# Optimization experiments

Hardware: AMD Instinct MI355X
Metric: run time of the kernel (lower is better)

Reference implementation:

```python
import jax, jax.numpy as jnp
import numpy as np

IOU_THRESHOLD = 0.5
NEG_POS_RATIO = 3
FOCAL_ALPHA = 0.25
FOCAL_GAMMA = 2.0
LOC_LOSS_WEIGHT = 1.0
EPS = 1e-7


def _make_boxes(key, shape):
    # valid xyxy boxes in [0,1]
    k1, k2 = jax.random.split(key)
    xy1 = jax.random.uniform(k1, shape[:-1] + (2,)) * 0.8
    wh = jax.random.uniform(k2, shape[:-1] + (2,)) * 0.2 + 0.01
    return jnp.concatenate([xy1, xy1 + wh], axis=-1)


def setup_inputs() -> dict:
    key = jax.random.key(0)
    k1, k2, k3 = jax.random.split(key, 3)
    B, A, G = 16, 65536, 64
    bbox_pred = _make_boxes(k1, (B, A, 4))
    conf_pred = jax.random.normal(k2, (B, A), dtype=jnp.float32)
    gt_boxes = _make_boxes(k3, (B, G, 4))
    return {"bbox_pred": bbox_pred, "conf_pred": conf_pred, "gt_boxes": gt_boxes}


def box_iou(a, b):
    # a: [A,4], b: [G,4] xyxy -> [A,G]
    area_a = (a[:, 2] - a[:, 0]) * (a[:, 3] - a[:, 1])
    area_b = (b[:, 2] - b[:, 0]) * (b[:, 3] - b[:, 1])
    lt = jnp.maximum(a[:, None, :2], b[None, :, :2])
    rb = jnp.minimum(a[:, None, 2:], b[None, :, 2:])
    wh = jnp.clip(rb - lt, 0.0)
    inter = wh[..., 0] * wh[..., 1]
    return inter / (area_a[:, None] + area_b[None, :] - inter + EPS)


def diou_loss(pred, gt):
    # pred, gt: [N,4] xyxy -> [N]
    area_p = (pred[:, 2] - pred[:, 0]) * (pred[:, 3] - pred[:, 1])
    area_g = (gt[:, 2] - gt[:, 0]) * (gt[:, 3] - gt[:, 1])
    lt = jnp.maximum(pred[:, :2], gt[:, :2])
    rb = jnp.minimum(pred[:, 2:], gt[:, 2:])
    wh = jnp.clip(rb - lt, 0.0)
    inter = wh[:, 0] * wh[:, 1]
    iou = inter / (area_p + area_g - inter + EPS)
    cp = (pred[:, :2] + pred[:, 2:]) * 0.5
    cg = (gt[:, :2] + gt[:, 2:]) * 0.5
    center_d2 = jnp.sum((cp - cg) ** 2, axis=-1)
    elt = jnp.minimum(pred[:, :2], gt[:, :2])
    erb = jnp.maximum(pred[:, 2:], gt[:, 2:])
    diag2 = jnp.sum((erb - elt) ** 2, axis=-1) + EPS
    return 1.0 - iou + center_d2 / diag2


def focal_loss(logits, targets):
    # BCE-with-logits, stable
    ce = jnp.maximum(logits, 0.0) - logits * targets + jnp.log1p(jnp.exp(-jnp.abs(logits)))
    p = jax.nn.sigmoid(logits)
    p_t = jnp.clip(p * targets + (1 - p) * (1 - targets), EPS, 1.0 - EPS)
    focal_w = jax.lax.stop_gradient((1.0 - p_t) ** FOCAL_GAMMA)
    alpha_t = FOCAL_ALPHA * targets + (1 - FOCAL_ALPHA) * (1 - targets)
    return alpha_t * focal_w * ce


def _per_image(bb, cp, gt):
    A = cp.shape[0]
    ious = box_iou(bb, gt)                     # [A,G]
    best_gt_iou = ious.max(axis=1)             # [A]
    best_gt_idx = ious.argmax(axis=1)          # [A]
    best_anchor_idx = ious.argmax(axis=0)      # [G]
    pos = best_gt_iou > IOU_THRESHOLD
    pos = pos.at[best_anchor_idx].set(True)    # force best anchor per GT positive
    posf = pos.astype(cp.dtype)
    num_pos = posf.sum()

    matched_gt = gt[best_gt_idx]               # [A,4]
    loc = (diou_loss(bb, matched_gt) * posf).sum() * LOC_LOSS_WEIGHT

    fl = focal_loss(cp, posf)                  # [A]
    pos_sum = (fl * posf).sum()
    # hard-negative mining: descending sort of negative losses, keep top k
    neg_vals = jnp.where(pos, -1.0, fl)        # focal loss >= 0, so -1 sentinel
    sorted_neg = -jnp.sort(-neg_vals)
    num_neg = jnp.minimum(A - num_pos, num_pos * NEG_POS_RATIO)
    keep = jnp.arange(A) < num_neg
    neg_sum = jnp.where(keep, sorted_neg, 0.0).sum()
    conf = (pos_sum + neg_sum) / jnp.maximum(num_pos + num_neg, 1.0)
    return loc, conf, num_pos


def reference(bbox_pred, conf_pred, gt_boxes):
    loc, conf, npos = jax.vmap(_per_image)(bbox_pred, conf_pred, gt_boxes)
    total_pos = jnp.maximum(npos.sum(), 1.0)
    avg_loc = loc.sum() / total_pos
    avg_conf = conf.sum() / total_pos
    return avg_loc + avg_conf, avg_conf, avg_loc
```

## Files before the change

kernel.cpp:

```cpp
#include <hip/hip_runtime.h>
#include <stdint.h>

#define A_N 65536
#define B_N 16
#define G_N 64
#define FEPS 1e-7f

#define NBIN 2048
#define SHB  21

__device__ __forceinline__ float focal_one(float l, float tt) {
  float e  = __expf(-fabsf(l));
  float sp = __logf(1.0f + e);
  bool  tp = tt > 0.5f;
  float ce = (tp ? fmaxf(-l, 0.0f) : fmaxf(l, 0.0f)) + sp;
  float inv = __builtin_amdgcn_rcpf(1.0f + e);
  float sig = (l >= 0.0f) ? inv : e * inv;
  float om  = tp ? (1.0f - sig) : sig;
  om = fminf(fmaxf(om, FEPS), 1.0f - FEPS);
  float alpha = tp ? 0.25f : 0.75f;
  return alpha * om * om * ce;
}

__device__ __forceinline__ float diou_one(float4 p, float4 q) {
  float ap = (p.z - p.x) * (p.w - p.y);
  float ag = (q.z - q.x) * (q.w - q.y);
  float ix1 = fmaxf(p.x, q.x), iy1 = fmaxf(p.y, q.y);
  float ix2 = fminf(p.z, q.z), iy2 = fminf(p.w, q.w);
  float iw = fmaxf(ix2 - ix1, 0.0f), ih = fmaxf(iy2 - iy1, 0.0f);
  float inter = iw * ih;
  float iou = inter / (ap + ag - inter + FEPS);
  float cpx = (p.x + p.z) * 0.5f, cpy = (p.y + p.w) * 0.5f;
  float cgx = (q.x + q.z) * 0.5f, cgy = (q.y + q.w) * 0.5f;
  float dx = cpx - cgx, dy = cpy - cgy;
  float cd2 = dx * dx + dy * dy;
  float ex1 = fminf(p.x, q.x), ey1 = fminf(p.y, q.y);
  float ex2 = fmaxf(p.z, q.z), ey2 = fmaxf(p.w, q.w);
  float ddx = ex2 - ex1, ddy = ey2 - ey1;
  float dg2 = ddx * ddx + ddy * ddy + FEPS;
  return 1.0f - iou + cd2 / dg2;
}

__global__ void dl_init(uint32_t* __restrict__ histz) {
  int i = blockIdx.x * 1024 + threadIdx.x;
  histz[i] = 0u;
}

__global__ __launch_bounds__(256) void dl_pass1(
    const float4* __restrict__ bbox, const float* __restrict__ conf,
    const float4* __restrict__ gt,
    uint8_t* __restrict__ best_idx, uint32_t* __restrict__ negkey,
    unsigned long long* __restrict__ gt_part,
    uint32_t* __restrict__ hist_cnt, float* __restrict__ hist_sum,
    float* __restrict__ part_loc, float* __restrict__ part_fl, float* __restrict__ part_np) {
  const int img = blockIdx.y;
  const int bx  = blockIdx.x;
  const int t   = threadIdx.x;
  const int wave = t >> 6, lane = t & 63;
  const int a = bx * 256 + t;
  const int idx = img * A_N + a;

  __shared__ float4 sg2[2 * G_N];
  __shared__ float  sga2[2 * G_N];
  __shared__ unsigned long long spart[4][G_N];
  __shared__ uint32_t hc[NBIN];
  __shared__ float    hs[NBIN];
  __shared__ float sl[4], sf[4], sn[4];

  for (int i = t; i < NBIN; i += 256) { hc[i] = 0u; hs[i] = 0.f; }
  if (t < G_N) {
    float4 q0 = gt[img * G_N + t];
    float qa0 = __fmul_rn(__fsub_rn(q0.z, q0.x), __fsub_rn(q0.w, q0.y));
    sg2[t] = q0;  sg2[t + G_N] = q0;
    sga2[t] = qa0; sga2[t + G_N] = qa0;
  }
  __syncthreads();

  float4 p = bbox[idx];
  float pa = __fmul_rn(__fsub_rn(p.z, p.x), __fsub_rn(p.w, p.y));
  float l = conf[idx];

  float posm = -1.f;
  uint32_t rowkey = 0u;
  uint32_t colkey = 0u;
  uint32_t tb = 63u - (uint32_t)lane;
  const int rotsrc = (lane + 1) & 63;
  const uint32_t lanecomp = 63u - (uint32_t)lane;

  #pragma unroll 8
  for (int j = 0; j < G_N; ++j) {
    float4 q = sg2[lane + j];
    float qa = sga2[lane + j];
    float ix1 = fmaxf(p.x, q.x), iy1 = fmaxf(p.y, q.y);
    float ix2 = fminf(p.z, q.z), iy2 = fminf(p.w, q.w);
    float iw = fmaxf(__fsub_rn(ix2, ix1), 0.f);
    float ih = fmaxf(__fsub_rn(iy2, iy1), 0.f);
    float inter = __fmul_rn(iw, ih);
    float den = __fadd_rn(__fsub_rn(__fadd_rn(pa, qa), inter), FEPS);
    posm = fmaxf(posm, __fmaf_rn(2.f, inter, -den));
    float ratio = inter * __builtin_amdgcn_rcpf(den);
    uint32_t base = __float_as_uint(ratio) & 0xFFFFFFC0u;
    uint32_t rkey = base | tb;
    if (rkey > rowkey) rowkey = rkey;
    uint32_t ckey = base | lanecomp;
    if (ckey > colkey) colkey = ckey;
    colkey = __shfl(colkey, rotsrc);
    tb = (tb - 1u) & 63u;
  }

  const bool pos = posm > 0.f;
  const int bidx = 63 - (int)(rowkey & 63u);
  best_idx[idx] = (uint8_t)bidx;

  float fl = focal_one(l, pos ? 1.0f : 0.0f);
  negkey[idx] = pos ? 0u : __float_as_uint(fl);
  float locv = pos ? diou_one(p, sg2[bidx]) : 0.0f;
  if (!pos) {
    uint32_t kb = __float_as_uint(fl);
    atomicAdd(&hc[kb >> SHB], 1u);
    atomicAdd(&hs[kb >> SHB], fl);
  }

  uint32_t winlane = 63u - (colkey & 63u);
  uint32_t ganchor = (uint32_t)(bx * 256 + wave * 64) + winlane;
  unsigned long long wkey = ((unsigned long long)(colkey & 0xFFFFFFC0u) << 32)
                          | (unsigned)~ganchor;
  spart[wave][lane] = wkey;

  float flp = pos ? fl : 0.0f;
  float np1 = pos ? 1.0f : 0.0f;
  float lv = locv;
  for (int o = 32; o; o >>= 1) {
    lv  += __shfl_down(lv, o);
    flp += __shfl_down(flp, o);
    np1 += __shfl_down(np1, o);
  }
  if (lane == 0) { sl[wave] = lv; sf[wave] = flp; sn[wave] = np1; }
  __syncthreads();

  for (int i = t; i < NBIN; i += 256) {
    uint32_t c = hc[i];
    if (c) {
      atomicAdd(&hist_cnt[img * NBIN + i], c);
      atomicAdd(&hist_sum[img * NBIN + i], hs[i]);
    }
  }
  if (t < G_N) {
    unsigned long long m = spart[0][t];
    if (spart[1][t] > m) m = spart[1][t];
    if (spart[2][t] > m) m = spart[2][t];
    if (spart[3][t] > m) m = spart[3][t];
    gt_part[(((size_t)(img << 8) | bx) << 6) | t] = m;
  }
  if (t == 0) {
    const int pi = img * 256 + bx;
    part_loc[pi] = sl[0] + sl[1] + sl[2] + sl[3];
    part_fl[pi]  = sf[0] + sf[1] + sf[2] + sf[3];
    part_np[pi]  = sn[0] + sn[1] + sn[2] + sn[3];
  }
}

__global__ __launch_bounds__(1024) void dl_select(
    uint32_t* negkey,
    const unsigned long long* __restrict__ gt_part,
    const uint32_t* __restrict__ hist_cnt, const float* __restrict__ hist_sum,
    const float* __restrict__ part_loc, const float* __restrict__ part_fl,
    const float* __restrict__ part_np,
    const float4* __restrict__ bbox, const float* __restrict__ conf,
    const float4* __restrict__ gt, const uint8_t* __restrict__ best_idx,
    float* __restrict__ acc) {
  const int img = blockIdx.x;
  const int t = threadIdx.x;
  uint32_t* negk = negkey + (size_t)img * A_N;
  const uint4* k4 = (const uint4*)negk;
  const int N4 = A_N / 4;

  __shared__ uint32_t cnt[NBIN];
  __shared__ float    bsum[NBIN];
  __shared__ uint32_t hc2[NBIN];
  __shared__ float    hs2[NBIN];
  __shared__ uint32_t cnt3[1024];
  __shared__ unsigned long long gred[16][G_N];
  __shared__ float s3[3][4];
  __shared__ float redf[16];
  __shared__ float np_sh, psum_sh, loc_sh, sstar_sh, sstar2_sh, negsum_sh;
  __shared__ float fix_l, fix_f, fix_n;
  __shared__ uint32_t bstar_sh, cstar_sh, b2_sh, c2_sh, j3_sh, c3_sh;

  for (int i = t; i < NBIN; i += 1024) {
    cnt[i]  = hist_cnt[img * NBIN + i];
    bsum[i] = hist_sum[img * NBIN + i];
    hc2[i] = 0u; hs2[i] = 0.f;
  }
  cnt3[t] = 0u;
  {
    const int g = t & 63, ch = t >> 6;
    unsigned long long m = 0ull;
    #pragma unroll 4
    for (int j = 0; j < 16; ++j) {
      unsigned long long v = gt_part[(((size_t)(img << 8) | (ch * 16 + j)) << 6) | g];
      if (v > m) m = v;
    }
    gred[ch][g] = m;
  }
  float lv = 0.f, fv = 0.f, nv = 0.f;
  if (t < 256) {
    lv = part_loc[img * 256 + t];
    fv = part_fl[img * 256 + t];
    nv = part_np[img * 256 + t];
  }
  for (int o = 32; o; o >>= 1) {
    lv += __shfl_down(lv, o);
    fv += __shfl_down(fv, o);
    nv += __shfl_down(nv, o);
  }
  if (t < 256 && (t & 63) == 0) { s3[0][t >> 6] = lv; s3[1][t >> 6] = fv; s3[2][t >> 6] = nv; }
  __syncthreads();

  if (t < 64) {
    unsigned long long m = gred[0][t];
    #pragma unroll
    for (int c = 1; c < 16; ++c) if (gred[c][t] > m) m = gred[c][t];
    uint32_t a = ~(uint32_t)(m & 0xFFFFFFFFull);
    uint32_t old = atomicExch(&negk[a], 0u);
    float dl = 0.f, df = 0.f, dn = 0.f;
    if (old != 0u) {
      dn = 1.f;
      float fln = __uint_as_float(old);
      uint32_t bin = old >> SHB;
      atomicSub(&cnt[bin], 1u);
      atomicAdd(&bsum[bin], -fln);
      const int ai = img * A_N + (int)a;
      df = focal_one(conf[ai], 1.0f);
      dl = diou_one(bbox[ai], gt[img * G_N + best_idx[ai]]);
    }
    for (int o = 32; o; o >>= 1) {
      dl += __shfl_down(dl, o);
      df += __shfl_down(df, o);
      dn += __shfl_down(dn, o);
    }
    if (t == 0) { fix_l = dl; fix_f = df; fix_n = dn; }
  }
  __syncthreads();

  if (t == 0) {
    loc_sh  = s3[0][0] + s3[0][1] + s3[0][2] + s3[0][3] + fix_l;
    psum_sh = s3[1][0] + s3[1][1] + s3[1][2] + s3[1][3] + fix_f;
    np_sh   = s3[2][0] + s3[2][1] + s3[2][2] + s3[2][3] + fix_n;
    negsum_sh = 0.f;
  }
  __syncthreads();

  const int np = (int)(np_sh + 0.5f);
  const int k = min(A_N - np, 3 * np);

  if (k > 0) {
    if (t < 64) {
      const int CH = NBIN / 64;
      const int lob = NBIN - CH * (t + 1);
      uint32_t csum = 0;
      for (int b = lob; b < lob + CH; ++b) csum += cnt[b];
      uint32_t pre = csum;
      for (int o = 1; o < 64; o <<= 1) { uint32_t u = __shfl_up(pre, o); if (t >= o) pre += u; }
      uint32_t run = pre - csum;
      for (int b = lob + CH - 1; b >= lob; --b) {
        uint32_t c = cnt[b];
        if (run < (uint32_t)k && run + c >= (uint32_t)k) { bstar_sh = (uint32_t)b; cstar_sh = run; }
        run += c;
      }
    }
    __syncthreads();
    const uint32_t bstar = bstar_sh;
    const uint32_t cbin = cnt[bstar];
    const uint32_t r = (uint32_t)k - cstar_sh;

    float s = 0.f;
    for (int i = t; i < NBIN; i += 1024) if (i > (int)bstar) s += bsum[i];
    for (int o = 32; o; o >>= 1) s += __shfl_down(s, o);
    if ((t & 63) == 0) redf[t >> 6] = s;
    __syncthreads();
    if (t == 0) {
      float ss = 0.f;
      #pragma unroll
      for (int w = 0; w < 16; ++w) ss += redf[w];
      sstar_sh = ss;
    }
    __syncthreads();

    if (r == cbin) {
      if (t == 0) negsum_sh = sstar_sh + bsum[bstar];
    } else {
      for (int i = t; i < N4; i += 1024) {
        uint4 v = k4[i];
        if (v.x != 0u && (v.x >> SHB) == bstar) { atomicAdd(&hc2[(v.x >> 10) & 2047u], 1u); atomicAdd(&hs2[(v.x >> 10) & 2047u], __uint_as_float(v.x)); }
        if (v.y != 0u && (v.y >> SHB) == bstar) { atomicAdd(&hc2[(v.y >> 10) & 2047u], 1u); atomicAdd(&hs2[(v.y >> 10) & 2047u], __uint_as_float(v.y)); }
        if (v.z != 0u && (v.z >> SHB) == bstar) { atomicAdd(&hc2[(v.z >> 10) & 2047u], 1u); atomicAdd(&hs2[(v.z >> 10) & 2047u], __uint_as_float(v.z)); }
        if (v.w != 0u && (v.w >> SHB) == bstar) { atomicAdd(&hc2[(v.w >> 10) & 2047u], 1u); atomicAdd(&hs2[(v.w >> 10) & 2047u], __uint_as_float(v.w)); }
      }
      __syncthreads();

      if (t < 64) {
        const int CH = NBIN / 64;
        const int lob = NBIN - CH * (t + 1);
        uint32_t csum = 0;
        for (int b = lob; b < lob + CH; ++b) csum += hc2[b];
        uint32_t pre = csum;
        for (int o = 1; o < 64; o <<= 1) { uint32_t u = __shfl_up(pre, o); if (t >= o) pre += u; }
        uint32_t run = pre - csum;
        for (int b = lob + CH - 1; b >= lob; --b) {
          uint32_t c = hc2[b];
          if (run < r && run + c >= r) { b2_sh = (uint32_t)b; c2_sh = run; }
          run += c;
        }
      }
      __syncthreads();
      const uint32_t b2 = b2_sh;
      const uint32_t cbin2 = hc2[b2];
      const uint32_t r3 = r - c2_sh;

      float s2 = 0.f;
      for (int i = t; i < NBIN; i += 1024) if (i > (int)b2) s2 += hs2[i];
      for (int o = 32; o; o >>= 1) s2 += __shfl_down(s2, o);
      if ((t & 63) == 0) redf[t >> 6] = s2;
      __syncthreads();
      if (t == 0) {
        float ss = 0.f;
        #pragma unroll
        for (int w = 0; w < 16; ++w) ss += redf[w];
        sstar2_sh = ss;
      }
      __syncthreads();

      if (r3 == cbin2) {
        if (t == 0) negsum_sh = sstar_sh + sstar2_sh + hs2[b2];
      } else {
        const uint32_t top22 = (bstar << 11) | b2;
        for (int i = t; i < N4; i += 1024) {
          uint4 v = k4[i];
          if (v.x != 0u && (v.x >> 10) == top22) atomicAdd(&cnt3[v.x & 1023u], 1u);
          if (v.y != 0u && (v.y >> 10) == top22) atomicAdd(&cnt3[v.y & 1023u], 1u);
          if (v.z != 0u && (v.z >> 10) == top22) atomicAdd(&cnt3[v.z & 1023u], 1u);
          if (v.w != 0u && (v.w >> 10) == top22) atomicAdd(&cnt3[v.w & 1023u], 1u);
        }
        __syncthreads();

        if (t < 64) {
          const int CH = 1024 / 64;
          const int lob = 1024 - CH * (t + 1);
          uint32_t csum = 0;
          for (int b = lob; b < lob + CH; ++b) csum += cnt3[b];
          uint32_t pre = csum;
          for (int o = 1; o < 64; o <<= 1) { uint32_t u = __shfl_up(pre, o); if (t >= o) pre += u; }
          uint32_t run = pre - csum;
          for (int b = lob + CH - 1; b >= lob; --b) {
            uint32_t c = cnt3[b];
            if (run < r3 && run + c >= r3) { j3_sh = (uint32_t)b; c3_sh = run; }
            run += c;
          }
        }
        __syncthreads();
        const uint32_t j3 = j3_sh;
        const uint32_t hibits = (bstar << SHB) | (b2 << 10);

        float s3v = 0.f;
        if (t > (int)j3 && cnt3[t]) {
          s3v = (float)cnt3[t] * __uint_as_float(hibits | (uint32_t)t);
        }
        for (int o = 32; o; o >>= 1) s3v += __shfl_down(s3v, o);
        if ((t & 63) == 0) redf[t >> 6] = s3v;
        __syncthreads();
        if (t == 0) {
          float ss = 0.f;
          #pragma unroll
          for (int w = 0; w < 16; ++w) ss += redf[w];
          negsum_sh = sstar_sh + sstar2_sh + ss
                    + (float)(int)(r3 - c3_sh) * __uint_as_float(hibits | j3);
        }
      }
    }
  }
  __syncthreads();
  if (t == 0) {
    acc[img] = loc_sh;
    acc[32 + img] = (float)np;
    acc[48 + img] = (psum_sh + negsum_sh) / fmaxf((float)(np + k), 1.0f);
  }
}

__global__ void dl_final(const float* __restrict__ acc, float* __restrict__ out) {
  if (threadIdx.x == 0 && blockIdx.x == 0) {
    float sl = 0.0f, sc = 0.0f, sn = 0.0f;
    for (int i = 0; i < B_N; ++i) {
      sl += acc[i];
      sc += acc[48 + i];
      sn += acc[32 + i];
    }
    float tp = fmaxf(sn, 1.0f);
    float al = sl / tp;
    float ac = sc / tp;
    out[0] = al + ac;
    out[1] = ac;
    out[2] = al;
  }
}

extern "C" void kernel_launch(void* const* d_in, const int* in_sizes, int n_in,
                              void* d_out, int out_size, void* d_ws, size_t ws_size,
                              hipStream_t stream) {
  (void)in_sizes; (void)n_in; (void)out_size; (void)ws_size;

  const float4* bbox = (const float4*)d_in[0];
  const float*  conf = (const float*)d_in[1];
  const float4* gt   = (const float4*)d_in[2];
  float* out = (float*)d_out;

  char* ws = (char*)d_ws;
  uint32_t*           negkey   = (uint32_t*)(ws);
  unsigned long long* gt_part  = (unsigned long long*)(ws + (4u << 20));
  uint8_t*            best_idx = (uint8_t*)(ws + (6u << 20));
  char* hb = ws + (7u << 20);
  uint32_t* hist_cnt = (uint32_t*)(hb);
  float*    hist_sum = (float*)(hb + (size_t)B_N * NBIN * 4);
  char* tail = hb + 2 * (size_t)B_N * NBIN * 4;
  float* part_loc = (float*)(tail);
  float* part_fl  = (float*)(tail + 16384);
  float* part_np  = (float*)(tail + 32768);
  float* acc      = (float*)(tail + 49152);

  dl_init<<<64, 1024, 0, stream>>>(hist_cnt );
  dl_pass1<<<dim3(A_N / 256, B_N), 256, 0, stream>>>(bbox, conf, gt, best_idx, negkey,
                                                     gt_part, hist_cnt, hist_sum,
                                                     part_loc, part_fl, part_np);
  dl_select<<<B_N, 1024, 0, stream>>>(negkey, gt_part, hist_cnt, hist_sum,
                                      part_loc, part_fl, part_np,
                                      bbox, conf, gt, best_idx, acc);
  dl_final<<<1, 64, 0, stream>>>(acc, out);
}
```

Baseline: 148.2 us.

## Rebalance radix-select bins and parallelize second-level prefix scan across block

Changes the second radix-select level from 11 to 13 bits (8192 bins) and the third from 10 to 8 bits, so the third pass over the keys is less often needed or touches fewer bins. The scan over the larger second-level histogram is split across all 1024 threads with a two-level chunk prefix sum instead of 64 threads walking serially. It also recomputes GT box areas inside the IoU loop instead of reading a shared array, and writes the key max updates as max() calls. The cost is more shared memory for the bigger histograms, which can lower occupancy, and a few extra ALU ops per IoU step.

```diff
diff --git a/kernel.cpp b/kernel.cpp
--- a/kernel.cpp
+++ b/kernel.cpp
@@ -8,6 +8,8 @@
 
 #define NBIN 2048
 #define SHB  21
+#define NB2  8192
+#define NB3  256
 
 __device__ __forceinline__ float focal_one(float l, float tt) {
   float e  = __expf(-fabsf(l));
@@ -61,7 +63,6 @@
   const int idx = img * A_N + a;
 
   __shared__ float4 sg2[2 * G_N];
-  __shared__ float  sga2[2 * G_N];
   __shared__ unsigned long long spart[4][G_N];
   __shared__ uint32_t hc[NBIN];
   __shared__ float    hs[NBIN];
@@ -70,9 +71,7 @@
   for (int i = t; i < NBIN; i += 256) { hc[i] = 0u; hs[i] = 0.f; }
   if (t < G_N) {
     float4 q0 = gt[img * G_N + t];
-    float qa0 = __fmul_rn(__fsub_rn(q0.z, q0.x), __fsub_rn(q0.w, q0.y));
     sg2[t] = q0;  sg2[t + G_N] = q0;
-    sga2[t] = qa0; sga2[t + G_N] = qa0;
   }
   __syncthreads();
 
@@ -90,7 +89,7 @@
   #pragma unroll 8
   for (int j = 0; j < G_N; ++j) {
     float4 q = sg2[lane + j];
-    float qa = sga2[lane + j];
+    float qa = __fmul_rn(__fsub_rn(q.z, q.x), __fsub_rn(q.w, q.y));
     float ix1 = fmaxf(p.x, q.x), iy1 = fmaxf(p.y, q.y);
     float ix2 = fminf(p.z, q.z), iy2 = fminf(p.w, q.w);
     float iw = fmaxf(__fsub_rn(ix2, ix1), 0.f);
@@ -100,10 +99,8 @@
     posm = fmaxf(posm, __fmaf_rn(2.f, inter, -den));
     float ratio = inter * __builtin_amdgcn_rcpf(den);
     uint32_t base = __float_as_uint(ratio) & 0xFFFFFFC0u;
-    uint32_t rkey = base | tb;
-    if (rkey > rowkey) rowkey = rkey;
-    uint32_t ckey = base | lanecomp;
-    if (ckey > colkey) colkey = ckey;
+    rowkey = max(rowkey, base | tb);
+    colkey = max(colkey, base | lanecomp);
     colkey = __shfl(colkey, rotsrc);
     tb = (tb - 1u) & 63u;
   }
@@ -177,9 +174,11 @@
 
   __shared__ uint32_t cnt[NBIN];
   __shared__ float    bsum[NBIN];
-  __shared__ uint32_t hc2[NBIN];
-  __shared__ float    hs2[NBIN];
-  __shared__ uint32_t cnt3[1024];
+  __shared__ uint32_t hc2[NB2];
+  __shared__ float    hs2[NB2];
+  __shared__ uint32_t cnt3[NB3];
+  __shared__ uint32_t chunks[1024];
+  __shared__ uint32_t pbase[64];
   __shared__ unsigned long long gred[16][G_N];
   __shared__ float s3[3][4];
   __shared__ float redf[16];
@@ -190,9 +189,9 @@
   for (int i = t; i < NBIN; i += 1024) {
     cnt[i]  = hist_cnt[img * NBIN + i];
     bsum[i] = hist_sum[img * NBIN + i];
-    hc2[i] = 0u; hs2[i] = 0.f;
-  }
-  cnt3[t] = 0u;
+  }
+  for (int i = t; i < NB2; i += 1024) { hc2[i] = 0u; hs2[i] = 0.f; }
+  if (t < NB3) cnt3[t] = 0u;
   {
     const int g = t & 63, ch = t >> 6;
     unsigned long long m = 0ull;
@@ -292,22 +291,35 @@
     } else {
       for (int i = t; i < N4; i += 1024) {
         uint4 v = k4[i];
-        if (v.x != 0u && (v.x >> SHB) == bstar) { atomicAdd(&hc2[(v.x >> 10) & 2047u], 1u); atomicAdd(&hs2[(v.x >> 10) & 2047u], __uint_as_float(v.x)); }
-        if (v.y != 0u && (v.y >> SHB) == bstar) { atomicAdd(&hc2[(v.y >> 10) & 2047u], 1u); atomicAdd(&hs2[(v.y >> 10) & 2047u], __uint_as_float(v.y)); }
-        if (v.z != 0u && (v.z >> SHB) == bstar) { atomicAdd(&hc2[(v.z >> 10) & 2047u], 1u); atomicAdd(&hs2[(v.z >> 10) & 2047u], __uint_as_float(v.z)); }
-        if (v.w != 0u && (v.w >> SHB) == bstar) { atomicAdd(&hc2[(v.w >> 10) & 2047u], 1u); atomicAdd(&hs2[(v.w >> 10) & 2047u], __uint_as_float(v.w)); }
-      }
-      __syncthreads();
-
+        if (v.x != 0u && (v.x >> SHB) == bstar) { atomicAdd(&hc2[(v.x >> 8) & (NB2-1)], 1u); atomicAdd(&hs2[(v.x >> 8) & (NB2-1)], __uint_as_float(v.x)); }
+        if (v.y != 0u && (v.y >> SHB) == bstar) { atomicAdd(&hc2[(v.y >> 8) & (NB2-1)], 1u); atomicAdd(&hs2[(v.y >> 8) & (NB2-1)], __uint_as_float(v.y)); }
+        if (v.z != 0u && (v.z >> SHB) == bstar) { atomicAdd(&hc2[(v.z >> 8) & (NB2-1)], 1u); atomicAdd(&hs2[(v.z >> 8) & (NB2-1)], __uint_as_float(v.z)); }
+        if (v.w != 0u && (v.w >> SHB) == bstar) { atomicAdd(&hc2[(v.w >> 8) & (NB2-1)], 1u); atomicAdd(&hs2[(v.w >> 8) & (NB2-1)], __uint_as_float(v.w)); }
+      }
+      __syncthreads();
+
+      {
+        const int cb = NB2 - 8 * (t + 1);
+        uint32_t cs = 0;
+        #pragma unroll
+        for (int j = 0; j < 8; ++j) cs += hc2[cb + j];
+        chunks[t] = cs;
+      }
+      __syncthreads();
       if (t < 64) {
-        const int CH = NBIN / 64;
-        const int lob = NBIN - CH * (t + 1);
-        uint32_t csum = 0;
-        for (int b = lob; b < lob + CH; ++b) csum += hc2[b];
-        uint32_t pre = csum;
+        uint32_t s16 = 0;
+        #pragma unroll 4
+        for (int j = 0; j < 16; ++j) s16 += chunks[t * 16 + j];
+        uint32_t pre = s16;
         for (int o = 1; o < 64; o <<= 1) { uint32_t u = __shfl_up(pre, o); if (t >= o) pre += u; }
-        uint32_t run = pre - csum;
-        for (int b = lob + CH - 1; b >= lob; --b) {
+        pbase[t] = pre - s16;
+      }
+      __syncthreads();
+      {
+        uint32_t run = pbase[t >> 4];
+        const int gb = (t >> 4) << 4;
+        for (int j = gb; j < t; ++j) run += chunks[j];
+        for (int b = NB2 - 8 * t - 1; b >= NB2 - 8 * (t + 1); --b) {
           uint32_t c = hc2[b];
           if (run < r && run + c >= r) { b2_sh = (uint32_t)b; c2_sh = run; }
           run += c;
@@ -319,7 +331,7 @@
       const uint32_t r3 = r - c2_sh;
 
       float s2 = 0.f;
-      for (int i = t; i < NBIN; i += 1024) if (i > (int)b2) s2 += hs2[i];
+      for (int i = t; i < NB2; i += 1024) if (i > (int)b2) s2 += hs2[i];
       for (int o = 32; o; o >>= 1) s2 += __shfl_down(s2, o);
       if ((t & 63) == 0) redf[t >> 6] = s2;
       __syncthreads();
@@ -334,19 +346,19 @@
       if (r3 == cbin2) {
         if (t == 0) negsum_sh = sstar_sh + sstar2_sh + hs2[b2];
       } else {
-        const uint32_t top22 = (bstar << 11) | b2;
+        const uint32_t top24 = (bstar << 13) | b2;
         for (int i = t; i < N4; i += 1024) {
           uint4 v = k4[i];
-          if (v.x != 0u && (v.x >> 10) == top22) atomicAdd(&cnt3[v.x & 1023u], 1u);
-          if (v.y != 0u && (v.y >> 10) == top22) atomicAdd(&cnt3[v.y & 1023u], 1u);
-          if (v.z != 0u && (v.z >> 10) == top22) atomicAdd(&cnt3[v.z & 1023u], 1u);
-          if (v.w != 0u && (v.w >> 10) == top22) atomicAdd(&cnt3[v.w & 1023u], 1u);
+          if (v.x != 0u && (v.x >> 8) == top24) atomicAdd(&cnt3[v.x & 255u], 1u);
+          if (v.y != 0u && (v.y >> 8) == top24) atomicAdd(&cnt3[v.y & 255u], 1u);
+          if (v.z != 0u && (v.z >> 8) == top24) atomicAdd(&cnt3[v.z & 255u], 1u);
+          if (v.w != 0u && (v.w >> 8) == top24) atomicAdd(&cnt3[v.w & 255u], 1u);
         }
         __syncthreads();
 
         if (t < 64) {
-          const int CH = 1024 / 64;
-          const int lob = 1024 - CH * (t + 1);
+          const int CH = NB3 / 64;
+          const int lob = NB3 - CH * (t + 1);
           uint32_t csum = 0;
           for (int b = lob; b < lob + CH; ++b) csum += cnt3[b];
           uint32_t pre = csum;
@@ -360,10 +372,10 @@
         }
         __syncthreads();
         const uint32_t j3 = j3_sh;
-        const uint32_t hibits = (bstar << SHB) | (b2 << 10);
+        const uint32_t hibits = (bstar << SHB) | (b2 << 8);
 
         float s3v = 0.f;
-        if (t > (int)j3 && cnt3[t]) {
+        if (t < NB3 && t > (int)j3 && cnt3[t]) {
           s3v = (float)cnt3[t] * __uint_as_float(hibits | (uint32_t)t);
         }
         for (int o = 32; o; o >>= 1) s3v += __shfl_down(s3v, o);
```

New measurement: 147.5 us. No clear change (-0.5%).
